# Kernel tuning notes

Hardware: AMD Instinct MI355X
Metric: run time of the kernel (lower is better)

## Reference

```python
import jax, jax.numpy as jnp
import numpy as np

DIM = 1024
HEADS = 16
HEAD_DIM = DIM // HEADS
BLOCK = 32
FEAT = 128
EPS = 1e-8


def setup_inputs() -> dict:
    key = jax.random.key(0)
    ks = jax.random.split(key, 5)
    b, n = 4, 4096
    x = jax.random.normal(ks[0], (b, n, DIM), dtype=jnp.float32)
    Wqkv = jax.random.normal(ks[1], (DIM, 3 * DIM), dtype=jnp.float32) / np.sqrt(DIM)
    proj = jax.random.normal(ks[2], (HEADS, HEAD_DIM, FEAT), dtype=jnp.float32) / np.sqrt(HEAD_DIM)
    Wout = jax.random.normal(ks[3], (DIM, DIM), dtype=jnp.float32) / np.sqrt(DIM)
    bout = jnp.zeros((DIM,), dtype=jnp.float32)
    return {"x": x, "Wqkv": Wqkv, "proj": proj, "Wout": Wout, "bout": bout}


def reference(x, Wqkv, proj, Wout, bout):
    b, n, d = x.shape
    h, dh = HEADS, HEAD_DIM
    nb = n // BLOCK
    qkv = x @ Wqkv                                    # [b, n, 3d]
    q, k, v = jnp.split(qkv, 3, axis=-1)
    # [b, h, nb, bs, dh]
    def to_blocks(t):
        return t.reshape(b, nb, BLOCK, h, dh).transpose(0, 3, 1, 2, 4)
    q, k, v = to_blocks(q), to_blocks(k), to_blocks(v)
    # per-head feature projection + elu feature map
    qf = jax.nn.elu(jnp.einsum('bhmsd,hdf->bhmsf', q, proj)) + 1.0
    kf = jax.nn.elu(jnp.einsum('bhmsd,hdf->bhmsf', k, proj)) + 1.0
    kv = jnp.einsum('bhmsf,bhmsd->bhmfd', kf, v)      # per-block kv state
    out = jnp.einsum('bhmsf,bhmfd->bhmsd', qf, kv)
    z = 1.0 / (jnp.einsum('bhmsf,bhmf->bhms', qf, kf.sum(axis=3)) + EPS)
    out = out * z[..., None]
    out = out.transpose(0, 2, 3, 1, 4).reshape(b, n, d)  # [b, n, d]
    return out @ Wout + bout
```

## Files before the change

### kernel.cpp

```cpp
#include <hip/hip_runtime.h>
#include <stdint.h>


typedef unsigned short u16;
typedef __attribute__((ext_vector_type(4))) float f32x4;
typedef __attribute__((ext_vector_type(8))) __bf16 bf16x8;
typedef __attribute__((ext_vector_type(8))) u16 us8;
typedef __attribute__((ext_vector_type(4))) u16 us4;

#define GLOAD_LDS16(g, l)                                                      \
  __builtin_amdgcn_global_load_lds(                                            \
      (const __attribute__((address_space(1))) void*)(g),                      \
      (__attribute__((address_space(3))) void*)(l), 16, 0, 0)

__device__ __forceinline__ u16 f2bf(float f) {
  union { float f; unsigned u; } x; x.f = f;
  return (u16)((x.u + 0x7fffu + ((x.u >> 16) & 1u)) >> 16);
}

__device__ __forceinline__ bf16x8 ld8(const void* p) {
  return __builtin_bit_cast(bf16x8, *(const us8*)p);
}

__device__ __forceinline__ f32x4 mfma16(bf16x8 a, bf16x8 b, f32x4 c) {
  return __builtin_amdgcn_mfma_f32_16x16x32_bf16(a, b, c, 0, 0, 0);
}

__global__ void cast_bf16_k(const float* __restrict__ in, u16* __restrict__ out,
                            int n4) {
  int stride = gridDim.x * blockDim.x;
  for (int i = blockIdx.x * blockDim.x + threadIdx.x; i < n4; i += stride) {
    f32x4 v = ((const f32x4*)in)[i];
    us4 o;
    o[0] = f2bf(v[0]); o[1] = f2bf(v[1]); o[2] = f2bf(v[2]); o[3] = f2bf(v[3]);
    ((us4*)out)[i] = o;
  }
}

__global__ __launch_bounds__(256)
void tcast_k(const float* __restrict__ in, u16* __restrict__ out, int R, int C) {
  __shared__ float tile[32][33];
  int tx = threadIdx.x & 31, ty = threadIdx.x >> 5;
  int r0 = blockIdx.y * 32, c0 = blockIdx.x * 32;
#pragma unroll
  for (int i = 0; i < 32; i += 8)
    tile[ty + i][tx] = in[(size_t)(r0 + ty + i) * C + c0 + tx];
  __syncthreads();
#pragma unroll
  for (int i = 0; i < 32; i += 8)
    out[(size_t)(c0 + ty + i) * R + r0 + tx] = f2bf(tile[tx][ty + i]);
}

__global__ __launch_bounds__(256)
void tcastv_k(const float* __restrict__ Wqkv, u16* __restrict__ dst) {
  __shared__ float tile[32][33];
  int tx = threadIdx.x & 31, ty = threadIdx.x >> 5;
  int e0 = blockIdx.y * 32, j0 = blockIdx.x * 32;
#pragma unroll
  for (int i = 0; i < 32; i += 8)
    tile[ty + i][tx] = Wqkv[(size_t)(e0 + ty + i) * 3072 + 2048 + j0 + tx];
  __syncthreads();
#pragma unroll
  for (int i = 0; i < 32; i += 8)
    dst[(size_t)(j0 + ty + i) * 1024 + e0 + tx] = f2bf(tile[tx][ty + i]);
}

__global__ __launch_bounds__(256)
void wqpb_k(const float* __restrict__ Wqkv, const float* __restrict__ proj,
            u16* __restrict__ BtAll) {
  __shared__ float pl[64][128];
  const int ec = blockIdx.x, h = blockIdx.y, qk = blockIdx.z;
  const float* ph = proj + (size_t)h * 8192;
  for (int i = threadIdx.x; i < 2048; i += 256)
    ((f32x4*)&pl[0][0])[i] = ((const f32x4*)ph)[i];
  __syncthreads();
  const int e = ec * 128 + (threadIdx.x >> 1);
  const int f0 = (threadIdx.x & 1) * 64;
  float wrow[64];
  const float* src = Wqkv + (size_t)e * 3072 + qk * 1024 + h * 64;
#pragma unroll
  for (int i = 0; i < 16; ++i)
    *(f32x4*)&wrow[i * 4] = *(const f32x4*)&src[i * 4];
  u16* dst = BtAll + (size_t)(qk * 2048 + h * 128) * 1024 + e;
  for (int fg = 0; fg < 16; ++fg) {
    f32x4 acc = (f32x4){0.f, 0.f, 0.f, 0.f};
    const int f = f0 + fg * 4;
#pragma unroll
    for (int d = 0; d < 64; ++d) {
      f32x4 p = *(f32x4*)&pl[d][f];
      acc += wrow[d] * p;
    }
#pragma unroll
    for (int u = 0; u < 4; ++u) dst[(size_t)(f + u) * 1024] = f2bf(acc[u]);
  }
}

template <int EPI>
__global__ __launch_bounds__(512, 1)
void gemm8p_k(const u16* __restrict__ A, int lda,
              const u16* __restrict__ Bt, int ldb,
              const float* __restrict__ bias,
              u16* __restrict__ o_qkf, u16* __restrict__ o_v,
              float* __restrict__ o_f32, int K, int ntx) {
  __shared__ __align__(16) char lds[131072];
  const int tid = threadIdx.x, lane = tid & 63, w = tid >> 6;
  const int wm = w >> 2, wn = w & 3;
  const int lr = lane & 15, lg = lane >> 4;
  const int cpx = (int)gridDim.x >> 3;
  const int bid = blockIdx.x;
  const int s = (bid & 7) * cpx + (bid >> 3);
  const int bxN = (s % ntx) * 256;
  const int byM = (s / ntx) * 256;
  const int nt = K >> 6;

  const int srow = w * 8 + (lane >> 3);
  const int scol = ((lane & 7) ^ ((lane >> 3) & 7)) * 8;

  auto stg = [&](const u16* src, int ld, int row0, int kt, int dstoff) {
#pragma unroll
    for (int j = 0; j < 2; ++j)
      GLOAD_LDS16(src + (size_t)(row0 + j * 64 + srow) * ld + kt + scol,
                  lds + dstoff + j * 8192 + w * 1024);
  };
  auto stgA0 = [&](int t) { stg(A, lda, byM, t * 64, (t & 1) * 65536); };
  auto stgA1 = [&](int t) { stg(A, lda, byM + 128, t * 64, (t & 1) * 65536 + 16384); };
  auto stgB0 = [&](int t) { stg(Bt, ldb, bxN, t * 64, (t & 1) * 65536 + 32768); };
  auto stgB1 = [&](int t) { stg(Bt, ldb, bxN + 128, t * 64, (t & 1) * 65536 + 49152); };

  f32x4 acc[8][4];
#pragma unroll
  for (int i = 0; i < 8; ++i)
#pragma unroll
    for (int j = 0; j < 4; ++j) acc[i][j] = (f32x4){0.f, 0.f, 0.f, 0.f};

  stgA0(0); stgA1(0); stgB0(0); stgB1(0);
  if (nt > 1) {
    stgB0(1); stgB1(1);
    asm volatile("s_waitcnt vmcnt(4)" ::: "memory");
  } else {
    asm volatile("s_waitcnt vmcnt(0)" ::: "memory");
  }
  __builtin_amdgcn_s_barrier();

  for (int t = 0; t < nt; ++t) {
    const char* Ab = lds + (t & 1) * 65536 + wm * 16384;
    const char* Bb = lds + (t & 1) * 65536 + 32768 + (wn >> 1) * 16384;
    const int brow = (wn & 1) * 64;
    bf16x8 alo[4][2], ahi[4][2], bl[4][2];

    if (t + 1 < nt) { stgA0(t + 1); stgA1(t + 1); }
#pragma unroll
    for (int i = 0; i < 4; ++i)
#pragma unroll
      for (int ks = 0; ks < 2; ++ks) {
        int row = i * 16 + lr;
        alo[i][ks] = ld8(Ab + row * 128 + ((ks * 64 + lg * 16) ^ ((row & 7) << 4)));
      }
#pragma unroll
    for (int j = 0; j < 4; ++j)
#pragma unroll
      for (int ks = 0; ks < 2; ++ks) {
        int row = brow + j * 16 + lr;
        bl[j][ks] = ld8(Bb + row * 128 + ((ks * 64 + lg * 16) ^ ((row & 7) << 4)));
      }
#pragma unroll
    for (int i = 0; i < 4; ++i)
#pragma unroll
      for (int j = 0; j < 4; ++j)
#pragma unroll
        for (int ks = 0; ks < 2; ++ks)
          acc[i][j] = mfma16(alo[i][ks], bl[j][ks], acc[i][j]);
    __builtin_amdgcn_s_barrier();

    if (t + 2 < nt) { stgB0(t + 2); stgB1(t + 2); }
#pragma unroll
    for (int i = 0; i < 4; ++i)
#pragma unroll
      for (int ks = 0; ks < 2; ++ks) {
        int row = (4 + i) * 16 + lr;
        ahi[i][ks] = ld8(Ab + row * 128 + ((ks * 64 + lg * 16) ^ ((row & 7) << 4)));
      }
#pragma unroll
    for (int i = 0; i < 4; ++i)
#pragma unroll
      for (int j = 0; j < 4; ++j)
#pragma unroll
        for (int ks = 0; ks < 2; ++ks)
          acc[4 + i][j] = mfma16(ahi[i][ks], bl[j][ks], acc[4 + i][j]);
    if (t < nt - 2)
      asm volatile("s_waitcnt vmcnt(4)" ::: "memory");
    else
      asm volatile("s_waitcnt vmcnt(0)" ::: "memory");
    __builtin_amdgcn_s_barrier();
  }

  const bool doelu = (EPI == 0) && (bxN < 4096);
#pragma unroll
  for (int mi = 0; mi < 8; ++mi)
#pragma unroll
    for (int nj = 0; nj < 4; ++nj) {
      const int col = bxN + wn * 64 + nj * 16 + lr;
#pragma unroll
      for (int rr = 0; rr < 4; ++rr) {
        const int row = byM + wm * 128 + mi * 16 + lg * 4 + rr;
        float x = acc[mi][nj][rr];
        if (EPI == 0) {
          if (doelu) {
            float v = x > 0.f ? x + 1.f : __expf(x);
            o_qkf[(size_t)row * 4096 + col] = f2bf(v);
          } else {
            o_v[(size_t)row * 1024 + (col - 4096)] = f2bf(x);
          }
        } else {
          o_f32[(size_t)row * 1024 + col] = x + bias[col];
        }
      }
    }
}

__global__ __launch_bounds__(64)
void attn_lite_k(const u16* __restrict__ qkf, u16* __restrict__ vbuf) {
  __shared__ __align__(16) u16 V_l[32 * 72];
  __shared__ __align__(16) u16 S_l[32 * 32];
  const int lane = threadIdx.x;
  const int bid = blockIdx.x;
  const int m = bid & 127, h = (bid >> 7) & 15, b = bid >> 11;
  const size_t t0 = (size_t)b * 4096 + (size_t)m * 32;
  const u16* qf = qkf + t0 * 4096 + h * 128;
  const u16* kf = qf + 2048;
  u16* vv = vbuf + t0 * 1024 + h * 64;
  const int lr = lane & 15, lg = lane >> 4;

#pragma unroll
  for (int it = 0; it < 4; ++it) {
    int s2 = it * 8 + (lane >> 3);
    int d0 = (lane & 7) * 8;
    *(us8*)&V_l[s2 * 72 + d0] = *(const us8*)&vv[(size_t)s2 * 1024 + d0];
  }

  f32x4 sacc[2][2];
#pragma unroll
  for (int mm = 0; mm < 2; ++mm)
#pragma unroll
    for (int nn = 0; nn < 2; ++nn) sacc[mm][nn] = (f32x4){0.f, 0.f, 0.f, 0.f};
#pragma unroll
  for (int ks = 0; ks < 4; ++ks) {
    bf16x8 aq[2], bk[2];
#pragma unroll
    for (int mm = 0; mm < 2; ++mm) {
      aq[mm] = ld8(&qf[(size_t)(mm * 16 + lr) * 4096 + ks * 32 + lg * 8]);
      bk[mm] = ld8(&kf[(size_t)(mm * 16 + lr) * 4096 + ks * 32 + lg * 8]);
    }
#pragma unroll
    for (int mm = 0; mm < 2; ++mm)
#pragma unroll
      for (int nn = 0; nn < 2; ++nn)
        sacc[mm][nn] = mfma16(aq[mm], bk[nn], sacc[mm][nn]);
  }

  float rs[2][4];
#pragma unroll
  for (int mm = 0; mm < 2; ++mm)
#pragma unroll
    for (int r = 0; r < 4; ++r) {
      float t = sacc[mm][0][r] + sacc[mm][1][r];
      t += __shfl_xor(t, 1);
      t += __shfl_xor(t, 2);
      t += __shfl_xor(t, 4);
      t += __shfl_xor(t, 8);
      rs[mm][r] = t;
    }

#pragma unroll
  for (int mm = 0; mm < 2; ++mm)
#pragma unroll
    for (int nn = 0; nn < 2; ++nn)
#pragma unroll
      for (int r = 0; r < 4; ++r) {
        int row = mm * 16 + lg * 4 + r;
        int byi = (nn * 16 + lr) * 2;
        *(u16*)((char*)S_l + row * 64 + (byi ^ ((row & 3) << 4))) =
            f2bf(sacc[mm][nn][r]);
      }

  bf16x8 vfr[4];
#pragma unroll
  for (int nn = 0; nn < 4; ++nn) {
    us8 g;
#pragma unroll
    for (int j = 0; j < 8; ++j) g[j] = V_l[(lg * 8 + j) * 72 + nn * 16 + lr];
    vfr[nn] = __builtin_bit_cast(bf16x8, g);
  }
  f32x4 pacc[2][4];
#pragma unroll
  for (int mm = 0; mm < 2; ++mm)
#pragma unroll
    for (int nn = 0; nn < 4; ++nn) pacc[mm][nn] = (f32x4){0.f, 0.f, 0.f, 0.f};
#pragma unroll
  for (int mm = 0; mm < 2; ++mm) {
    int row = mm * 16 + lr;
    int byi = lg * 16;
    bf16x8 a = ld8((char*)S_l + row * 64 + (byi ^ ((row & 3) << 4)));
#pragma unroll
    for (int nn = 0; nn < 4; ++nn) pacc[mm][nn] = mfma16(a, vfr[nn], pacc[mm][nn]);
  }

#pragma unroll
  for (int mm = 0; mm < 2; ++mm)
#pragma unroll
    for (int r = 0; r < 4; ++r) {
      float z = 1.f / (rs[mm][r] + 1e-8f);
      int q = mm * 16 + lg * 4 + r;
#pragma unroll
      for (int nn = 0; nn < 4; ++nn)
        vv[(size_t)q * 1024 + nn * 16 + lr] = f2bf(pacc[mm][nn][r] * z);
    }
}

extern "C" void kernel_launch(void* const* d_in, const int* in_sizes, int n_in,
                              void* d_out, int out_size, void* d_ws,
                              size_t ws_size, hipStream_t stream) {
  const float* x = (const float*)d_in[0];
  const float* Wqkv = (const float*)d_in[1];
  const float* proj = (const float*)d_in[2];
  const float* Wout = (const float*)d_in[3];
  const float* bout = (const float*)d_in[4];
  float* out = (float*)d_out;

  char* ws = (char*)d_ws;
  char* doc = (char*)d_out;

  u16* xb    = (u16*)doc;
  u16* btall = (u16*)(doc + 33554432);
  u16* qkf   = (u16*)ws;
  u16* vbuf  = (u16*)(ws + 134217728);
  u16* woutT = (u16*)(ws + 167772160);

  cast_bf16_k<<<2048, 256, 0, stream>>>(x, xb, 4194304);
  tcastv_k<<<dim3(32, 32), 256, 0, stream>>>(Wqkv, btall + (size_t)4096 * 1024);
  wqpb_k<<<dim3(8, 16, 2), 256, 0, stream>>>(Wqkv, proj, btall);
  tcast_k<<<dim3(32, 32), 256, 0, stream>>>(Wout, woutT, 1024, 1024);

  gemm8p_k<0><<<1280, 512, 0, stream>>>(xb, 1024, btall, 1024, nullptr,
                                        qkf, vbuf, nullptr, 1024, 20);

  attn_lite_k<<<8192, 64, 0, stream>>>(qkf, vbuf);

  gemm8p_k<1><<<256, 512, 0, stream>>>(vbuf, 1024, woutT, 1024, bout,
                                       nullptr, nullptr, out, 1024, 4);
}
```

Baseline: 418.3 us.

## Stage GEMM epilogue through LDS and write qk features in block-contiguous layout

The QKV GEMM epilogue now writes bf16 results into swizzled LDS first, then emits 16-byte vectorized global stores instead of scattered 2-byte stores. The q/k feature output is also rearranged into a per-(block, head, q/k) contiguous layout, so the attention kernel reads compact 128-element rows instead of rows strided by 4096. The cost is one extra barrier and an LDS round trip. It also relies on the LDS buffer being large enough to hold the full 256x256 bf16 tile.

```diff
diff --git a/kernel.cpp b/kernel.cpp
--- a/kernel.cpp
+++ b/kernel.cpp
@@ -194,41 +194,73 @@
     __builtin_amdgcn_s_barrier();
   }
 
-  const bool doelu = (EPI == 0) && (bxN < 4096);
+  if (EPI == 1) {
+#pragma unroll
+    for (int mi = 0; mi < 8; ++mi)
+#pragma unroll
+      for (int nj = 0; nj < 4; ++nj) {
+        const int col = bxN + wn * 64 + nj * 16 + lr;
+        const float bia = bias[col];
+#pragma unroll
+        for (int rr = 0; rr < 4; ++rr) {
+          const int row = byM + wm * 128 + mi * 16 + lg * 4 + rr;
+          o_f32[(size_t)row * 1024 + col] = acc[mi][nj][rr] + bia;
+        }
+      }
+    return;
+  }
+
+  const bool doelu = (bxN < 4096);
+  u16* cl = (u16*)lds;
 #pragma unroll
   for (int mi = 0; mi < 8; ++mi)
 #pragma unroll
-    for (int nj = 0; nj < 4; ++nj) {
-      const int col = bxN + wn * 64 + nj * 16 + lr;
+    for (int nj = 0; nj < 4; ++nj)
 #pragma unroll
       for (int rr = 0; rr < 4; ++rr) {
-        const int row = byM + wm * 128 + mi * 16 + lg * 4 + rr;
-        float x = acc[mi][nj][rr];
-        if (EPI == 0) {
-          if (doelu) {
-            float v = x > 0.f ? x + 1.f : __expf(x);
-            o_qkf[(size_t)row * 4096 + col] = f2bf(v);
-          } else {
-            o_v[(size_t)row * 1024 + (col - 4096)] = f2bf(x);
-          }
-        } else {
-          o_f32[(size_t)row * 1024 + col] = x + bias[col];
-        }
-      }
-    }
+        const int rl = wm * 128 + mi * 16 + lg * 4 + rr;
+        const int clm = wn * 64 + nj * 16 + lr;
+        float xv = acc[mi][nj][rr];
+        float v = doelu ? (xv > 0.f ? xv + 1.f : __expf(xv)) : xv;
+        *(u16*)((char*)cl + ((rl * 512 + clm * 2) ^ ((rl & 7) << 4))) = f2bf(v);
+      }
+  __syncthreads();
+  if (doelu) {
+#pragma unroll
+    for (int it = 0; it < 16; ++it) {
+      const int chunk = it * 512 + tid;
+      const int r = chunk >> 5, g = (chunk >> 4) & 1, k8 = chunk & 15;
+      us8 val = *(us8*)((char*)cl + ((r * 512 + g * 256 + k8 * 16) ^ ((r & 7) << 4)));
+      const int token = byM + r;
+      const int cg = bxN + g * 128;
+      const int qk = cg >> 11;
+      const int h = (cg >> 7) & 15;
+      const size_t dst =
+          ((((size_t)(token >> 5) * 16 + h) * 2 + qk) * 32 + (token & 31)) * 128 +
+          k8 * 8;
+      *(us8*)&o_qkf[dst] = val;
+    }
+  } else {
+#pragma unroll
+    for (int it = 0; it < 16; ++it) {
+      const int chunk = it * 512 + tid;
+      const int r = chunk >> 5, k = chunk & 31;
+      us8 val = *(us8*)((char*)cl + ((r * 512 + k * 16) ^ ((r & 7) << 4)));
+      *(us8*)&o_v[(size_t)(byM + r) * 1024 + (bxN - 4096) + k * 8] = val;
+    }
+  }
 }
 
 __global__ __launch_bounds__(64)
-void attn_lite_k(const u16* __restrict__ qkf, u16* __restrict__ vbuf) {
+void attn_lite_k(const u16* __restrict__ qkfB, u16* __restrict__ vbuf) {
   __shared__ __align__(16) u16 V_l[32 * 72];
   __shared__ __align__(16) u16 S_l[32 * 32];
   const int lane = threadIdx.x;
   const int bid = blockIdx.x;
-  const int m = bid & 127, h = (bid >> 7) & 15, b = bid >> 11;
-  const size_t t0 = (size_t)b * 4096 + (size_t)m * 32;
-  const u16* qf = qkf + t0 * 4096 + h * 128;
-  const u16* kf = qf + 2048;
-  u16* vv = vbuf + t0 * 1024 + h * 64;
+  const int h = bid & 15, mglob = bid >> 4;
+  const u16* qf = qkfB + (size_t)mglob * 131072 + h * 8192;
+  const u16* kf = qf + 4096;
+  u16* vv = vbuf + (size_t)mglob * 32 * 1024 + h * 64;
   const int lr = lane & 15, lg = lane >> 4;
 
 #pragma unroll
@@ -248,8 +280,8 @@
     bf16x8 aq[2], bk[2];
 #pragma unroll
     for (int mm = 0; mm < 2; ++mm) {
-      aq[mm] = ld8(&qf[(size_t)(mm * 16 + lr) * 4096 + ks * 32 + lg * 8]);
-      bk[mm] = ld8(&kf[(size_t)(mm * 16 + lr) * 4096 + ks * 32 + lg * 8]);
+      aq[mm] = ld8(&qf[(mm * 16 + lr) * 128 + ks * 32 + lg * 8]);
+      bk[mm] = ld8(&kf[(mm * 16 + lr) * 128 + ks * 32 + lg * 8]);
     }
 #pragma unroll
     for (int mm = 0; mm < 2; ++mm)
@@ -332,7 +364,7 @@
 
   u16* xb    = (u16*)doc;
   u16* btall = (u16*)(doc + 33554432);
-  u16* qkf   = (u16*)ws;
+  u16* qkfB  = (u16*)ws;
   u16* vbuf  = (u16*)(ws + 134217728);
   u16* woutT = (u16*)(ws + 167772160);
 
@@ -342,9 +374,9 @@
   tcast_k<<<dim3(32, 32), 256, 0, stream>>>(Wout, woutT, 1024, 1024);
 
   gemm8p_k<0><<<1280, 512, 0, stream>>>(xb, 1024, btall, 1024, nullptr,
-                                        qkf, vbuf, nullptr, 1024, 20);
-
-  attn_lite_k<<<8192, 64, 0, stream>>>(qkf, vbuf);
+                                        qkfB, vbuf, nullptr, 1024, 20);
+
+  attn_lite_k<<<8192, 64, 0, stream>>>(qkfB, vbuf);
 
   gemm8p_k<1><<<256, 512, 0, stream>>>(vbuf, 1024, woutT, 1024, bout,
                                        nullptr, nullptr, out, 1024, 4);
```

Result: no change. 414.6 us (-0.9%).
